# Optimization experiments

Hardware: AMD Instinct MI355X
Metric: run time of the kernel (lower is better)

Reference implementation:

```python
import jax, jax.numpy as jnp
from jax import lax
import numpy as np

B, N, NPOINT, NSAMPLE, RADIUS = 8, 16384, 1024, 32, 0.4
C_IN = 64


def fps(xyz, npoint):
    """Furthest point sampling. xyz: (B, N, 3) -> (B, npoint) int32 indices.
    Matches the CUDA kernel: start from index 0, iteratively pick argmax of
    the running min-distance to the selected set."""
    Bb, Nn, _ = xyz.shape

    def step(carry, _):
        min_d, last = carry
        p = jnp.take_along_axis(xyz, last[:, None, None], axis=1)  # (B,1,3)
        d = jnp.sum((xyz - p) ** 2, axis=-1)                       # (B,N)
        min_d = jnp.minimum(min_d, d)
        nxt = jnp.argmax(min_d, axis=1).astype(jnp.int32)
        return (min_d, nxt), nxt

    idx0 = jnp.zeros((Bb,), jnp.int32)
    min_d0 = jnp.full((Bb, Nn), jnp.inf, xyz.dtype)
    _, rest = lax.scan(step, (min_d0, idx0), None, length=npoint - 1)  # (npoint-1, B)
    return jnp.transpose(jnp.concatenate([idx0[None, :], rest], axis=0))  # (B, npoint)


def ball_query(xyz, new_xyz, radius, nsample):
    """xyz: (B,N,3), new_xyz: (B,P,3) -> (B,P,nsample) int32 indices.
    First nsample in-radius indices (ascending), short balls padded with the
    first found index (the centroid itself is always in-radius)."""
    Nn = xyz.shape[1]
    d2 = jnp.sum((new_xyz[:, :, None, :] - xyz[:, None, :, :]) ** 2, axis=-1)  # (B,P,N)
    ar = jnp.arange(Nn, dtype=jnp.int32)
    key = jnp.where(d2 <= radius * radius, ar, Nn)  # out-of-ball -> sentinel N
    neg_top, _ = lax.top_k(-key, nsample)           # nsample smallest keys
    gidx = -neg_top                                  # (B,P,nsample)
    return jnp.where(gidx == Nn, gidx[..., :1], gidx)


def setup_inputs() -> dict:
    key = jax.random.key(0)
    ks = jax.random.split(key, 8)
    return {
        "xyz": jax.random.normal(ks[0], (B, N, 3), jnp.float32),
        "features": jax.random.normal(ks[1], (B, C_IN, N), jnp.float32),
        "W1": jax.random.normal(ks[2], (64, 3 + C_IN), jnp.float32) * 0.05,
        "b1": jax.random.normal(ks[3], (64,), jnp.float32) * 0.05,
        "W2": jax.random.normal(ks[4], (64, 64), jnp.float32) * 0.05,
        "b2": jax.random.normal(ks[5], (64,), jnp.float32) * 0.05,
        "W3": jax.random.normal(ks[6], (128, 64), jnp.float32) * 0.05,
        "b3": jax.random.normal(ks[7], (128,), jnp.float32) * 0.05,
    }


def reference(xyz, features, W1, b1, W2, b2, W3, b3):
    Bb = xyz.shape[0]
    idx = fps(xyz, NPOINT)                                         # (B,P)
    new_xyz = jnp.take_along_axis(xyz, idx[:, :, None], axis=1)    # (B,P,3)

    gidx = ball_query(xyz, new_xyz, RADIUS, NSAMPLE)               # (B,P,S)
    bi = jnp.arange(Bb)[:, None, None]
    grouped_xyz = xyz[bi, gidx] - new_xyz[:, :, None, :]           # (B,P,S,3) relative coords
    feats_t = jnp.transpose(features, (0, 2, 1))                   # (B,N,C)
    grouped_feats = feats_t[bi, gidx]                              # (B,P,S,C)
    h = jnp.concatenate([grouped_xyz, grouped_feats], axis=-1)     # (B,P,S,3+C)

    # shared per-point MLP (1x1 convs) + ReLU
    h = jax.nn.relu(jnp.einsum('bpsc,oc->bpso', h, W1) + b1)
    h = jax.nn.relu(jnp.einsum('bpsc,oc->bpso', h, W2) + b2)
    h = jax.nn.relu(jnp.einsum('bpsc,oc->bpso', h, W3) + b3)

    pooled = jnp.max(h, axis=2)                                    # (B,P,128) max over nsample
    new_features = jnp.transpose(pooled, (0, 2, 1))                # (B,128,P)
    return new_xyz, new_features
```

## Files before the change

### kernel.cpp

```cpp
#include <hip/hip_runtime.h>

#define R2 0.16f

typedef float f32x2 __attribute__((ext_vector_type(2)));

__device__ __forceinline__ float sqd(float x, float y, float z,
                                     float px, float py, float pz) {
  float dx = __fsub_rn(x, px);
  float dy = __fsub_rn(y, py);
  float dz = __fsub_rn(z, pz);
  return __fadd_rn(__fadd_rn(__fmul_rn(dx, dx), __fmul_rn(dy, dy)),
                   __fmul_rn(dz, dz));
}

__device__ __forceinline__ float wave64_max_dpp(float x) {
#define DPP_STEP(CTRL)                                                      \
  {                                                                         \
    int t_ = __builtin_amdgcn_update_dpp(__float_as_int(x),                 \
                                         __float_as_int(x), CTRL, 0xf, 0xf, \
                                         false);                            \
    x = fmaxf(x, __int_as_float(t_));                                       \
  }
  DPP_STEP(0x111) DPP_STEP(0x112) DPP_STEP(0x114)
  DPP_STEP(0x118) DPP_STEP(0x142) DPP_STEP(0x143)
#undef DPP_STEP
  return x;
}
__device__ __forceinline__ unsigned wave64_min_dpp_u32(unsigned x) {
#define DPP_STEP(CTRL)                                                      \
  {                                                                         \
    unsigned t_ = (unsigned)__builtin_amdgcn_update_dpp(                    \
        (int)x, (int)x, CTRL, 0xf, 0xf, false);                             \
    x = (t_ < x) ? t_ : x;                                                  \
  }
  DPP_STEP(0x111) DPP_STEP(0x112) DPP_STEP(0x114)
  DPP_STEP(0x118) DPP_STEP(0x142) DPP_STEP(0x143)
#undef DPP_STEP
  return x;
}

__global__ __launch_bounds__(256) void zero_hist(unsigned* __restrict__ h) {
  h[blockIdx.x * 256 + threadIdx.x] = 0u;
}

__global__ __launch_bounds__(256) void hist_kernel(const float* __restrict__ xyz,
                                                   unsigned* __restrict__ hist,
                                                   unsigned* __restrict__ rank,
                                                   unsigned* __restrict__ cid) {
  int t = blockIdx.x * 256 + threadIdx.x;
  int b = t >> 14;
  const float* p = xyz + (size_t)t * 3;
  int cx = (int)floorf(p[0] + 4.0f);
  int cy = (int)floorf(p[1] + 4.0f);
  int cz = (int)floorf(p[2] + 4.0f);
  cx = min(max(cx, 0), 7);
  cy = min(max(cy, 0), 7);
  cz = min(max(cz, 0), 7);
  unsigned c = (unsigned)(cx | (cy << 3) | (cz << 6));
  unsigned r = atomicAdd(&hist[(b << 9) + c], 1u);
  rank[t] = r;
  cid[t] = c;
}

__global__ __launch_bounds__(512) void scan_kernel(const unsigned* __restrict__ hist,
                                                   unsigned* __restrict__ starts) {
  __shared__ unsigned a[512];
  int b = blockIdx.x, t = threadIdx.x;
  unsigned h = hist[(b << 9) + t];
  a[t] = h;
  __syncthreads();
  for (int s = 1; s < 512; s <<= 1) {
    unsigned v = (t >= s) ? a[t - s] : 0u;
    __syncthreads();
    a[t] += v;
    __syncthreads();
  }
  starts[(b << 9) + t] = a[t] - h;
}

__global__ __launch_bounds__(256) void scatter_kernel(
    const float* __restrict__ xyz, const unsigned* __restrict__ starts,
    const unsigned* __restrict__ rank, const unsigned* __restrict__ cid,
    float* __restrict__ xs2, float* __restrict__ ys2, float* __restrict__ zs2,
    unsigned* __restrict__ oi2) {
  int t = blockIdx.x * 256 + threadIdx.x;
  int b = t >> 14, n = t & 16383;
  unsigned pos = starts[(b << 9) + cid[t]] + rank[t];
  const float* p = xyz + (size_t)t * 3;
  size_t o = ((size_t)b << 14) + pos;
  xs2[o] = p[0];
  ys2[o] = p[1];
  zs2[o] = p[2];
  oi2[o] = (unsigned)n;
}

__global__ __launch_bounds__(1024) void fps_kernel(
    const float* __restrict__ xyz, const float* __restrict__ xs,
    const float* __restrict__ ys, const float* __restrict__ zs,
    const unsigned* __restrict__ oi, int* __restrict__ idx_out) {
#pragma clang fp contract(off)
  extern __shared__ float4 xylds[];
  __shared__ unsigned s_wval[2][16];
  __shared__ unsigned s_woi[2][16];
  int b = blockIdx.x;
  int tid = threadIdx.x;
  int lane = tid & 63, wid = tid >> 6;
  const float* xb = xyz + (size_t)b * 16384 * 3;
  int base = tid << 4;
  const float4* xv = (const float4*)(xs + ((size_t)b << 14) + base);
  const float4* yv = (const float4*)(ys + ((size_t)b << 14) + base);
  const float4* zv = (const float4*)(zs + ((size_t)b << 14) + base);
  const uint4* ov = (const uint4*)(oi + ((size_t)b << 14) + base);
  float xr[16], yr[16], zr[16];
  unsigned OI[16];
#pragma unroll
  for (int q = 0; q < 4; ++q) {
    *(float4*)(xr + 4 * q) = xv[q];
    *(float4*)(yr + 4 * q) = yv[q];
    *(float4*)(zr + 4 * q) = zv[q];
    *(uint4*)(OI + 4 * q) = ov[q];
  }
  float bxl = xr[0], bxh = xr[0], byl = yr[0], byh = yr[0], bzl = zr[0],
        bzh = zr[0];
#pragma unroll
  for (int k = 1; k < 16; ++k) {
    bxl = fminf(bxl, xr[k]); bxh = fmaxf(bxh, xr[k]);
    byl = fminf(byl, yr[k]); byh = fmaxf(byh, yr[k]);
    bzl = fminf(bzl, zr[k]); bzh = fmaxf(bzh, zr[k]);
  }
  f32x2 Z[8], M[8];
#pragma unroll
  for (int q = 0; q < 8; ++q) {
    xylds[(q << 10) + tid] =
        make_float4(xr[2 * q], xr[2 * q + 1], yr[2 * q], yr[2 * q + 1]);
    Z[q] = {zr[2 * q], zr[2 * q + 1]};
    M[q] = {__builtin_inff(), __builtin_inff()};
  }
  if (tid == 0) idx_out[b * 1024] = 0;
  __syncthreads();
  float px = xb[0], py = xb[1], pz = xb[2];
  float tv = __builtin_inff();
  for (int it = 1; it < 1024; ++it) {
    int sl = it & 1;
    float ddx = fmaxf(fmaxf(bxl - px, px - bxh), 0.0f);
    float ddy = fmaxf(fmaxf(byl - py, py - byh), 0.0f);
    float ddz = fmaxf(fmaxf(bzl - pz, pz - bzh), 0.0f);
    float lb = (ddx * ddx + ddy * ddy + ddz * ddz) * 0.999f;
    if (lb < tv) {
      f32x2 px2 = {px, px}, py2 = {py, py}, pz2 = {pz, pz};
      float ntv = -1.0f;
#pragma unroll
      for (int q = 0; q < 8; ++q) {
        float4 t = xylds[(q << 10) + tid];
        f32x2 X = {t.x, t.y};
        f32x2 Y = {t.z, t.w};
        f32x2 dx = X - px2;
        f32x2 dy = Y - py2;
        f32x2 dz = Z[q] - pz2;
        f32x2 d = dx * dx + dy * dy + dz * dz;
        M[q].x = fminf(M[q].x, d.x);
        M[q].y = fminf(M[q].y, d.y);
        ntv = fmaxf(fmaxf(ntv, M[q].x), M[q].y);
      }
      tv = ntv;
    }
    float bv = wave64_max_dpp(tv);
    unsigned bvb = (unsigned)__builtin_amdgcn_readlane(__float_as_int(bv), 63);
    float bvf = __int_as_float((int)bvb);
    unsigned coi = 0xffffffffu;
    if (tv == bvf) {
#pragma unroll
      for (int q = 0; q < 8; ++q) {
        if (M[q].x == bvf && OI[2 * q] < coi) coi = OI[2 * q];
        if (M[q].y == bvf && OI[2 * q + 1] < coi) coi = OI[2 * q + 1];
      }
    }
    unsigned woi = wave64_min_dpp_u32(coi);
    if (lane == 63) {
      s_wval[sl][wid] = bvb;
      s_woi[sl][wid] = woi;
    }
    __syncthreads();
    unsigned w0 = s_wval[sl][lane & 15];
    unsigned o0 = s_woi[sl][lane & 15];
    unsigned v = w0;
#pragma unroll
    for (int off = 1; off <= 8; off <<= 1) {
      unsigned ov_ = __shfl_xor(v, off);
      v = (ov_ > v) ? ov_ : v;
    }
    unsigned cand = (w0 == v) ? o0 : 0xffffffffu;
#pragma unroll
    for (int off = 1; off <= 8; off <<= 1) {
      unsigned oc = __shfl_xor(cand, off);
      cand = (oc < cand) ? oc : cand;
    }
    int j = (int)cand;
    if (tid == 0) idx_out[b * 1024 + it] = j;
    px = xb[j * 3 + 0];
    py = xb[j * 3 + 1];
    pz = xb[j * 3 + 2];
  }
}

__global__ __launch_bounds__(256) void gather_newxyz(const float* __restrict__ xyz,
                                                     const int* __restrict__ idx,
                                                     float* __restrict__ out) {
  int t = blockIdx.x * 256 + threadIdx.x;
  int b = t >> 10;
  int i = idx[t];
  const float* src = xyz + ((size_t)b * 16384 + i) * 3;
  float* dst = out + (size_t)t * 3;
  dst[0] = src[0];
  dst[1] = src[1];
  dst[2] = src[2];
}

__global__ __launch_bounds__(256) void transpose_feats(const float* __restrict__ f,
                                                       float* __restrict__ fT) {
  __shared__ float tile[64][65];
  int b = blockIdx.x >> 8;
  int n0 = (blockIdx.x & 255) << 6;
  int t = threadIdx.x;
  int nn = t & 63, c0 = t >> 6;
#pragma unroll
  for (int r = 0; r < 64; r += 4) {
    int c = c0 + r;
    tile[c][nn] = f[((size_t)b * 64 + c) * 16384 + n0 + nn];
  }
  __syncthreads();
  int cc = t & 63, n1 = t >> 6;
#pragma unroll
  for (int r = 0; r < 64; r += 4) {
    int n = n1 + r;
    fT[((size_t)b * 16384 + n0 + n) * 64 + cc] = tile[cc][n];
  }
}

__global__ __launch_bounds__(256) void ballquery_kernel(const float* __restrict__ xyz,
                                                        const float* __restrict__ newxyz,
                                                        int* __restrict__ gidx) {
  int wid = threadIdx.x >> 6, lane = threadIdx.x & 63;
  int cid = blockIdx.x * 4 + wid;
  int b = cid >> 10;
  const float* xb = xyz + (size_t)b * 16384 * 3;
  float cx = newxyz[cid * 3 + 0];
  float cy = newxyz[cid * 3 + 1];
  float cz = newxyz[cid * 3 + 2];
  int* out = gidx + (size_t)cid * 32;
  int found = 0;
  int first = -1;
  for (int c0 = 0; c0 < 16384; c0 += 64) {
    int g = c0 + lane;
    float xx = xb[g * 3 + 0], yy = xb[g * 3 + 1], zz = xb[g * 3 + 2];
    float d2 = sqd(xx, yy, zz, cx, cy, cz);
    bool inr = (d2 <= R2);
    unsigned long long mask = __ballot(inr);
    if (first < 0 && mask) first = c0 + (int)__builtin_ctzll(mask);
    int pre = __popcll(mask & ((1ull << lane) - 1ull));
    int slot = found + pre;
    if (inr && slot < 32) out[slot] = g;
    found += __popcll(mask);
    if (found >= 32) break;
  }
  for (int s = found + lane; s < 32; s += 64) out[s] = first;
}

#define FMA16(BASEPTR)                                                     \
  do {                                                                     \
    const float4* hp_ = (const float4*)(BASEPTR);                          \
    float4 v0 = hp_[0], v1 = hp_[1], v2 = hp_[2], v3 = hp_[3];             \
    float a = acc[s];                                                      \
    a = fmaf(w[0], v0.x, a);  a = fmaf(w[1], v0.y, a);                     \
    a = fmaf(w[2], v0.z, a);  a = fmaf(w[3], v0.w, a);                     \
    a = fmaf(w[4], v1.x, a);  a = fmaf(w[5], v1.y, a);                     \
    a = fmaf(w[6], v1.z, a);  a = fmaf(w[7], v1.w, a);                     \
    a = fmaf(w[8], v2.x, a);  a = fmaf(w[9], v2.y, a);                     \
    a = fmaf(w[10], v2.z, a); a = fmaf(w[11], v2.w, a);                    \
    a = fmaf(w[12], v3.x, a); a = fmaf(w[13], v3.y, a);                    \
    a = fmaf(w[14], v3.z, a); a = fmaf(w[15], v3.w, a);                    \
    acc[s] = a;                                                            \
  } while (0)

__global__ __launch_bounds__(256) void mlp_kernel(
    const float* __restrict__ xyz, const float* __restrict__ feats,
    const float* __restrict__ featsT, const float* __restrict__ newxyz,
    const int* __restrict__ gidx,
    const float* __restrict__ W1, const float* __restrict__ b1,
    const float* __restrict__ W2, const float* __restrict__ b2,
    const float* __restrict__ W3, const float* __restrict__ b3,
    float* __restrict__ out, int useT) {
  __shared__ float buf[4][32 * 68];
  int wid = threadIdx.x >> 6, lane = threadIdx.x & 63;
  int cid = blockIdx.x * 4 + wid;
  int b = cid >> 10, p = cid & 1023;
  float* A = buf[wid];
  const int* gi = gidx + (size_t)cid * 32;
  float cx = newxyz[cid * 3 + 0];
  float cy = newxyz[cid * 3 + 1];
  float cz = newxyz[cid * 3 + 2];

  if (useT) {
    const float4* fT4 = (const float4*)(featsT + (size_t)b * 16384 * 64);
    for (int t = lane; t < 512; t += 64) {
      int s = t >> 4, q = t & 15;
      int g = gi[s];
      float4 v = fT4[(size_t)g * 16 + q];
      *(float4*)(A + s * 68 + q * 4) = v;
    }
  } else {
    const float* fb = feats + (size_t)b * 64 * 16384;
    for (int t = lane; t < 2048; t += 64) {
      int c = t >> 5, s = t & 31;
      int g = gi[s];
      A[s * 68 + c] = fb[(size_t)c * 16384 + g];
    }
  }
  for (int t = lane; t < 96; t += 64) {
    int s = t / 3, c = t - s * 3;
    int g = gi[s];
    float pv = xyz[((size_t)b * 16384 + g) * 3 + c];
    float cv = (c == 0) ? cx : ((c == 1) ? cy : cz);
    A[s * 68 + 64 + c] = __fsub_rn(pv, cv);
  }
  if (lane < 32) A[lane * 68 + 67] = 0.0f;
  __syncthreads();

  int o = lane;
  float acc[32];

#pragma unroll
  for (int s = 0; s < 32; ++s) acc[s] = b1[o];
  {
    const float* wr = W1 + o * 67;
    for (int cb = 0; cb < 4; ++cb) {
      float w[16];
#pragma unroll
      for (int q = 0; q < 16; ++q) w[q] = wr[3 + cb * 16 + q];
#pragma unroll
      for (int s = 0; s < 32; ++s) { FMA16(A + s * 68 + cb * 16); }
    }
    float w0 = wr[0], w1 = wr[1], w2 = wr[2];
#pragma unroll
    for (int s = 0; s < 32; ++s) {
      float a = acc[s];
      a = fmaf(w0, A[s * 68 + 64], a);
      a = fmaf(w1, A[s * 68 + 65], a);
      a = fmaf(w2, A[s * 68 + 66], a);
      acc[s] = a;
    }
  }
  __syncthreads();
#pragma unroll
  for (int s = 0; s < 32; ++s) A[s * 64 + o] = fmaxf(acc[s], 0.0f);
  __syncthreads();

#pragma unroll
  for (int s = 0; s < 32; ++s) acc[s] = b2[o];
  {
    const float* wr = W2 + o * 64;
    for (int cb = 0; cb < 4; ++cb) {
      float w[16];
#pragma unroll
      for (int q = 0; q < 16; ++q) w[q] = wr[cb * 16 + q];
#pragma unroll
      for (int s = 0; s < 32; ++s) { FMA16(A + s * 64 + cb * 16); }
    }
  }
  __syncthreads();
#pragma unroll
  for (int s = 0; s < 32; ++s) A[s * 64 + o] = fmaxf(acc[s], 0.0f);
  __syncthreads();

  float* outp = out + 24576;
  for (int po = 0; po < 2; ++po) {
    int o2 = lane + (po << 6);
#pragma unroll
    for (int s = 0; s < 32; ++s) acc[s] = b3[o2];
    const float* wr = W3 + o2 * 64;
    for (int cb = 0; cb < 4; ++cb) {
      float w[16];
#pragma unroll
      for (int q = 0; q < 16; ++q) w[q] = wr[cb * 16 + q];
#pragma unroll
      for (int s = 0; s < 32; ++s) { FMA16(A + s * 64 + cb * 16); }
    }
    float mx = 0.0f;
#pragma unroll
    for (int s = 0; s < 32; ++s) mx = fmaxf(mx, acc[s]);
    outp[((size_t)b * 128 + o2) * 1024 + p] = mx;
  }
}

extern "C" void kernel_launch(void* const* d_in, const int* in_sizes, int n_in,
                              void* d_out, int out_size, void* d_ws, size_t ws_size,
                              hipStream_t stream) {
  const float* xyz = (const float*)d_in[0];
  const float* feats = (const float*)d_in[1];
  const float* W1 = (const float*)d_in[2];
  const float* b1 = (const float*)d_in[3];
  const float* W2 = (const float*)d_in[4];
  const float* b2 = (const float*)d_in[5];
  const float* W3 = (const float*)d_in[6];
  const float* b3 = (const float*)d_in[7];
  float* out = (float*)d_out;

  char* w = (char*)d_ws;
  int* idx = (int*)w;
  int* gidx = (int*)(w + 32768);
  unsigned* hist = (unsigned*)(w + 1081344);
  unsigned* starts = (unsigned*)(w + 1097728);
  unsigned* rank = (unsigned*)(w + 1114112);
  unsigned* cid = (unsigned*)(w + 1638400);
  unsigned* oi2 = (unsigned*)(w + 2162688);
  float* xs2 = (float*)(w + 2686976);
  float* ys2 = (float*)(w + 3211264);
  float* zs2 = (float*)(w + 3735552);
  float* featsT = (float*)(w + 4259840);
  size_t needT = 4259840 + (size_t)8 * 16384 * 64 * sizeof(float);
  int useT = (ws_size >= needT) ? 1 : 0;

  zero_hist<<<16, 256, 0, stream>>>(hist);
  hist_kernel<<<512, 256, 0, stream>>>(xyz, hist, rank, cid);
  scan_kernel<<<8, 512, 0, stream>>>(hist, starts);
  scatter_kernel<<<512, 256, 0, stream>>>(xyz, starts, rank, cid, xs2, ys2,
                                          zs2, oi2);
  fps_kernel<<<8, 1024, 131072, stream>>>(xyz, xs2, ys2, zs2, oi2, idx);
  gather_newxyz<<<32, 256, 0, stream>>>(xyz, idx, out);
  if (useT) transpose_feats<<<2048, 256, 0, stream>>>(feats, featsT);
  ballquery_kernel<<<2048, 256, 0, stream>>>(xyz, out, gidx);
  mlp_kernel<<<2048, 256, 0, stream>>>(xyz, feats, featsT, out, gidx,
                                       W1, b1, W2, b2, W3, b3, out, useT);
}
```

Measured before the change: 2.203 ms.

## Halve FPS block size, use LDS atomic key reduction and broadcast winner coords

```diff
diff --git a/kernel.cpp b/kernel.cpp
--- a/kernel.cpp
+++ b/kernel.cpp
@@ -94,27 +94,27 @@
   oi2[o] = (unsigned)n;
 }
 
-__global__ __launch_bounds__(1024) void fps_kernel(
+__global__ __launch_bounds__(512) void fps_kernel(
     const float* __restrict__ xyz, const float* __restrict__ xs,
     const float* __restrict__ ys, const float* __restrict__ zs,
     const unsigned* __restrict__ oi, int* __restrict__ idx_out) {
 #pragma clang fp contract(off)
   extern __shared__ float4 xylds[];
-  __shared__ unsigned s_wval[2][16];
-  __shared__ unsigned s_woi[2][16];
+  __shared__ unsigned long long s_gkey[3];
+  __shared__ float s_cd[3][3][8];
   int b = blockIdx.x;
   int tid = threadIdx.x;
   int lane = tid & 63, wid = tid >> 6;
   const float* xb = xyz + (size_t)b * 16384 * 3;
-  int base = tid << 4;
+  int base = tid << 5;
   const float4* xv = (const float4*)(xs + ((size_t)b << 14) + base);
   const float4* yv = (const float4*)(ys + ((size_t)b << 14) + base);
   const float4* zv = (const float4*)(zs + ((size_t)b << 14) + base);
   const uint4* ov = (const uint4*)(oi + ((size_t)b << 14) + base);
-  float xr[16], yr[16], zr[16];
-  unsigned OI[16];
-#pragma unroll
-  for (int q = 0; q < 4; ++q) {
+  float xr[32], yr[32], zr[32];
+  unsigned OI[32];
+#pragma unroll
+  for (int q = 0; q < 8; ++q) {
     *(float4*)(xr + 4 * q) = xv[q];
     *(float4*)(yr + 4 * q) = yv[q];
     *(float4*)(zr + 4 * q) = zv[q];
@@ -123,25 +123,27 @@
   float bxl = xr[0], bxh = xr[0], byl = yr[0], byh = yr[0], bzl = zr[0],
         bzh = zr[0];
 #pragma unroll
-  for (int k = 1; k < 16; ++k) {
+  for (int k = 1; k < 32; ++k) {
     bxl = fminf(bxl, xr[k]); bxh = fmaxf(bxh, xr[k]);
     byl = fminf(byl, yr[k]); byh = fmaxf(byh, yr[k]);
     bzl = fminf(bzl, zr[k]); bzh = fmaxf(bzh, zr[k]);
   }
-  f32x2 Z[8], M[8];
-#pragma unroll
-  for (int q = 0; q < 8; ++q) {
-    xylds[(q << 10) + tid] =
+  f32x2 Z[16], M[16];
+#pragma unroll
+  for (int q = 0; q < 16; ++q) {
+    xylds[(q << 9) + tid] =
         make_float4(xr[2 * q], xr[2 * q + 1], yr[2 * q], yr[2 * q + 1]);
     Z[q] = {zr[2 * q], zr[2 * q + 1]};
     M[q] = {__builtin_inff(), __builtin_inff()};
   }
   if (tid == 0) idx_out[b * 1024] = 0;
+  if (tid < 3) s_gkey[tid] = 0ull;
   __syncthreads();
   float px = xb[0], py = xb[1], pz = xb[2];
   float tv = __builtin_inff();
   for (int it = 1; it < 1024; ++it) {
-    int sl = it & 1;
+    int sl = it % 3;
+    int slp2 = (sl + 2) % 3;
     float ddx = fmaxf(fmaxf(bxl - px, px - bxh), 0.0f);
     float ddy = fmaxf(fmaxf(byl - py, py - byh), 0.0f);
     float ddz = fmaxf(fmaxf(bzl - pz, pz - bzh), 0.0f);
@@ -150,8 +152,8 @@
       f32x2 px2 = {px, px}, py2 = {py, py}, pz2 = {pz, pz};
       float ntv = -1.0f;
 #pragma unroll
-      for (int q = 0; q < 8; ++q) {
-        float4 t = xylds[(q << 10) + tid];
+      for (int q = 0; q < 16; ++q) {
+        float4 t = xylds[(q << 9) + tid];
         f32x2 X = {t.x, t.y};
         f32x2 Y = {t.z, t.w};
         f32x2 dx = X - px2;
@@ -168,38 +170,38 @@
     unsigned bvb = (unsigned)__builtin_amdgcn_readlane(__float_as_int(bv), 63);
     float bvf = __int_as_float((int)bvb);
     unsigned coi = 0xffffffffu;
+    float wx = 0.0f, wy = 0.0f, wz = 0.0f;
     if (tv == bvf) {
 #pragma unroll
-      for (int q = 0; q < 8; ++q) {
-        if (M[q].x == bvf && OI[2 * q] < coi) coi = OI[2 * q];
-        if (M[q].y == bvf && OI[2 * q + 1] < coi) coi = OI[2 * q + 1];
+      for (int q = 0; q < 16; ++q) {
+        float4 t = xylds[(q << 9) + tid];
+        if (M[q].x == bvf && OI[2 * q] < coi) {
+          coi = OI[2 * q]; wx = t.x; wy = t.z; wz = Z[q].x;
+        }
+        if (M[q].y == bvf && OI[2 * q + 1] < coi) {
+          coi = OI[2 * q + 1]; wx = t.y; wy = t.w; wz = Z[q].y;
+        }
       }
     }
     unsigned woi = wave64_min_dpp_u32(coi);
-    if (lane == 63) {
-      s_wval[sl][wid] = bvb;
-      s_woi[sl][wid] = woi;
+    if (coi == woi && coi != 0xffffffffu) {
+      s_cd[sl][0][wid] = wx;
+      s_cd[sl][1][wid] = wy;
+      s_cd[sl][2][wid] = wz;
+      unsigned long long key = ((unsigned long long)bvb << 17) |
+                               ((unsigned long long)(16383u - woi) << 3) |
+                               (unsigned long long)wid;
+      atomicMax(&s_gkey[sl], key);
     }
     __syncthreads();
-    unsigned w0 = s_wval[sl][lane & 15];
-    unsigned o0 = s_woi[sl][lane & 15];
-    unsigned v = w0;
-#pragma unroll
-    for (int off = 1; off <= 8; off <<= 1) {
-      unsigned ov_ = __shfl_xor(v, off);
-      v = (ov_ > v) ? ov_ : v;
-    }
-    unsigned cand = (w0 == v) ? o0 : 0xffffffffu;
-#pragma unroll
-    for (int off = 1; off <= 8; off <<= 1) {
-      unsigned oc = __shfl_xor(cand, off);
-      cand = (oc < cand) ? oc : cand;
-    }
-    int j = (int)cand;
+    unsigned long long gk = s_gkey[sl];
+    if (tid == 0) s_gkey[slp2] = 0ull;
+    int w2 = (int)(gk & 7ull);
+    int j = 16383 - (int)((gk >> 3) & 0x3fffull);
+    px = s_cd[sl][0][w2];
+    py = s_cd[sl][1][w2];
+    pz = s_cd[sl][2][w2];
     if (tid == 0) idx_out[b * 1024 + it] = j;
-    px = xb[j * 3 + 0];
-    py = xb[j * 3 + 1];
-    pz = xb[j * 3 + 2];
   }
 }
 
@@ -425,7 +427,7 @@
   scan_kernel<<<8, 512, 0, stream>>>(hist, starts);
   scatter_kernel<<<512, 256, 0, stream>>>(xyz, starts, rank, cid, xs2, ys2,
                                           zs2, oi2);
-  fps_kernel<<<8, 1024, 131072, stream>>>(xyz, xs2, ys2, zs2, oi2, idx);
+  fps_kernel<<<8, 512, 131072, stream>>>(xyz, xs2, ys2, zs2, oi2, idx);
   gather_newxyz<<<32, 256, 0, stream>>>(xyz, idx, out);
   if (useT) transpose_feats<<<2048, 256, 0, stream>>>(feats, featsT);
   ballquery_kernel<<<2048, 256, 0, stream>>>(xyz, out, gidx);
```

New measurement: 2.976 ms. 35.1% more time.
